# Kernel tuning notes

Hardware: AMD Instinct MI355X
Metric: run time of the kernel (lower is better)

## Reference

```python
import jax, jax.numpy as jnp
import numpy as np

N, F = 10000, 64
EDGE_PROB = 0.003  # sparse 0/1 adjacency, stored dense as in the original
LEAKY_SLOPE = 0.01
ELU_ALPHA = 1.0


def setup_inputs() -> dict:
    key = jax.random.key(0)
    ks = jax.random.split(key, 8)
    x = jax.random.normal(ks[0], (N, F), dtype=jnp.float32)
    # symmetric 0/1 adjacency (edge_index was concatenated with its flip)
    u = jax.random.uniform(ks[1], (N, N))
    A = (u < EDGE_PROB).astype(jnp.float32)
    A = jnp.maximum(A, A.T)
    dims = [F, 16, 32, 16, 32, 8]
    Ws = [jax.random.normal(ks[2 + i], (dims[i], dims[i + 1]), dtype=jnp.float32)
          * (1.0 / np.sqrt(dims[i])) for i in range(5)]
    return {"x": x, "A": A, "W0": Ws[0], "W1": Ws[1], "W2": Ws[2], "W3": Ws[3], "W4": Ws[4]}


def reference(x, A, W0, W1, W2, W3, W4):
    # layer s: temp = A @ h ; ahw = temp @ W[s] ; h = act(ahw)
    t1 = A @ x
    a1 = t1 @ W0
    h1 = jax.nn.relu(a1)

    t2 = A @ h1
    a2 = t2 @ W1
    h2 = jax.nn.silu(a2)  # swish

    t3 = A @ h2
    a3 = t3 @ W2
    h3 = jax.nn.elu(a3, alpha=ELU_ALPHA)

    t4 = A @ h3
    a4 = t4 @ W3
    h4 = jnp.where(a4 >= 0, a4, LEAKY_SLOPE * a4)  # leaky relu

    t5 = A @ h4
    a5 = t5 @ W4
    z = jax.nn.sigmoid(a5)

    # original returns (ah, ahw, z); flatten the lists into a tuple
    return (t1, t2, t3, t4, t5, a1, a2, a3, a4, a5, z)
```

## Files before the change

### kernel.cpp

```cpp
#include <hip/hip_runtime.h>
#include <math.h>

#define N_NODES 10000
#define NCH 40
#define NQ4 2500
#define CAPR 128
#define WCAP 64

typedef float f32x4 __attribute__((ext_vector_type(4)));

template <int ACT>
__device__ __forceinline__ float activate(float v) {
    if (ACT == 0) return fmaxf(v, 0.0f);
    if (ACT == 1) return v / (1.0f + __expf(-v));
    if (ACT == 2) return (v >= 0.0f) ? v : (__expf(v) - 1.0f);
    if (ACT == 3) return (v >= 0.0f) ? v : 0.01f * v;
    return 1.0f / (1.0f + __expf(-v));
}

__global__ __launch_bounds__(256) void scan_upper(
        const float* __restrict__ A,
        int* __restrict__ cu, int* __restrict__ colsU, int* __restrict__ cl) {
    __shared__ int sidx[4][WCAP];
    __shared__ int scnt[4];

    const int w    = threadIdx.x >> 6;
    const int lane = threadIdx.x & 63;
    const int row  = blockIdx.x;
    const int c0   = row >> 8;
    const int lo   = row & 255;

    const f32x4* __restrict__ arow = (const f32x4*)(A + (size_t)row * N_NODES);

    int cnt = 0;
    int c = c0 + w;
    f32x4 vc = (f32x4)(0.0f);
    if (c < NCH) {
        const int idx = c * 64 + lane;
        if (idx < NQ4) vc = __builtin_nontemporal_load(&arow[idx]);
    }
    while (c < NCH) {
        const int cn = c + 4;
        f32x4 vn = (f32x4)(0.0f);
        if (cn < NCH) {
            const int idxn = cn * 64 + lane;
            if (idxn < NQ4) vn = __builtin_nontemporal_load(&arow[idxn]);
        }
        if (c == c0) {
#pragma unroll
            for (int cc = 0; cc < 4; ++cc)
                if (4 * lane + cc < lo) vc[cc] = 0.0f;
        }
#pragma unroll
        for (int cc = 0; cc < 4; ++cc) {
            unsigned long long m = __ballot(vc[cc] != 0.0f);
            while (m) {
                const int b = __ffsll(m) - 1;
                m &= m - 1ull;
                if (lane == 0 && cnt < WCAP)
                    sidx[w][cnt] = 256 * c + 4 * b + cc;
                ++cnt;
            }
        }
        vc = vn;
        c = cn;
    }
    if (cnt > WCAP) cnt = WCAP;
    if (lane == 0) scnt[w] = cnt;
    __syncthreads();

    const int s0 = scnt[0], s1 = scnt[1], s2 = scnt[2], s3 = scnt[3];
    const int offs[4] = {0, s0, s0 + s1, s0 + s1 + s2};
    int total = s0 + s1 + s2 + s3;
    if (total > CAPR) total = CAPR;
    if (lane < scnt[w]) {
        const int p = offs[w] + lane;
        if (p < CAPR) colsU[row * CAPR + p] = sidx[w][lane];
    }
    if (threadIdx.x == 0) {
        cu[row] = total;
        cl[row] = 0;
    }
}

__global__ __launch_bounds__(256) void invert_upper(
        const int* __restrict__ cu, const int* __restrict__ colsU,
        int* __restrict__ cl, int* __restrict__ colsL) {
    const int w    = threadIdx.x >> 6;
    const int lane = threadIdx.x & 63;
    const int row  = blockIdx.x * 4 + w;

    const int n = cu[row];
    for (int k = lane; k < n; k += 64) {
        const int tgt = colsU[row * CAPR + k];
        if (tgt != row) {
            const int pos = atomicAdd(&cl[tgt], 1);
            if (pos < CAPR) colsL[tgt * CAPR + pos] = row;
        }
    }
}

__global__ __launch_bounds__(256) void sort_lower(
        int* __restrict__ cl, int* __restrict__ colsL) {
    __shared__ int sl[4][128];
    const int w    = threadIdx.x >> 6;
    const int lane = threadIdx.x & 63;
    const int row  = blockIdx.x * 4 + w;

    int n = cl[row];
    if (n > CAPR) n = CAPR;
    sl[w][lane]      = (lane < n)      ? colsL[row * CAPR + lane]      : 0x7FFFFFFF;
    sl[w][lane + 64] = (lane + 64 < n) ? colsL[row * CAPR + lane + 64] : 0x7FFFFFFF;
    __syncthreads();

    for (int size = 2; size <= 128; size <<= 1) {
        for (int stride = size >> 1; stride > 0; stride >>= 1) {
            const int i = ((lane & ~(stride - 1)) << 1) | (lane & (stride - 1));
            const int j = i | stride;
            const int a = sl[w][i], b = sl[w][j];
            const bool asc = (i & size) == 0;
            const bool doswap = asc ? (a > b) : (a < b);
            if (doswap) { sl[w][i] = b; sl[w][j] = a; }
            __syncthreads();
        }
    }

    if (lane < n)      colsL[row * CAPR + lane]      = sl[w][lane];
    if (lane + 64 < n) colsL[row * CAPR + lane + 64] = sl[w][lane + 64];
    if (lane == 0) cl[row] = n;
}

template <int FIN, int FOUT, int ACT>
__global__ __launch_bounds__(256) void layer_fused(
        const int* __restrict__ cl, const int* __restrict__ colsL,
        const int* __restrict__ cu, const int* __restrict__ colsU,
        const float* __restrict__ h_in, const float* __restrict__ W,
        float* __restrict__ t_out, float* __restrict__ a_out,
        float* __restrict__ h_out) {
    constexpr int G = 64 / FIN;
    __shared__ float tls[4][FIN];
    const int w    = threadIdx.x >> 6;
    const int lane = threadIdx.x & 63;
    const int row  = blockIdx.x * 4 + w;

    const int f = lane % FIN;
    const int g = lane / FIN;
    const int dl = cl[row];
    const int du = cu[row];
    const int* __restrict__ crowL = colsL + row * CAPR;
    const int* __restrict__ crowU = colsU + row * CAPR;

    float acc = 0.0f;
#pragma unroll 4
    for (int k = g; k < dl; k += G)
        acc += h_in[crowL[k] * FIN + f];
#pragma unroll 4
    for (int k = g; k < du; k += G)
        acc += h_in[crowU[k] * FIN + f];
#pragma unroll
    for (int off = FIN; off < 64; off <<= 1)
        acc += __shfl_xor(acc, off);
    if (g == 0) {
        t_out[row * FIN + f] = acc;
        tls[w][f] = acc;
    }
    __syncthreads();

    constexpr int NQP = 64 / FOUT;
    constexpr int K   = FIN / NQP;
    const int o = lane % FOUT, q = lane / FOUT;
    float a = 0.0f;
#pragma unroll
    for (int i = 0; i < K; ++i) {
        const int ff = q * K + i;
        a += tls[w][ff] * W[ff * FOUT + o];
    }
#pragma unroll
    for (int off = FOUT; off < 64; off <<= 1)
        a += __shfl_xor(a, off);
    if (q == 0) {
        a_out[row * FOUT + o] = a;
        h_out[row * FOUT + o] = activate<ACT>(a);
    }
}

extern "C" void kernel_launch(void* const* d_in, const int* in_sizes, int n_in,
                              void* d_out, int out_size, void* d_ws, size_t ws_size,
                              hipStream_t stream) {
    const float* x  = (const float*)d_in[0];
    const float* A  = (const float*)d_in[1];
    const float* W0 = (const float*)d_in[2];
    const float* W1 = (const float*)d_in[3];
    const float* W2 = (const float*)d_in[4];
    const float* W3 = (const float*)d_in[5];
    const float* W4 = (const float*)d_in[6];

    float* out = (float*)d_out;
    float* t1 = out + 0;
    float* t2 = out + 640000;
    float* t3 = out + 800000;
    float* t4 = out + 1120000;
    float* t5 = out + 1280000;
    float* a1 = out + 1600000;
    float* a2 = out + 1760000;
    float* a3 = out + 2080000;
    float* a4 = out + 2240000;
    float* a5 = out + 2560000;
    float* z  = out + 2640000;

    char* ws = (char*)d_ws;
    int*   cu    = (int*)ws;
    int*   cl    = (int*)(ws + (size_t)1 * 1024 * 1024);
    int*   colsU = (int*)(ws + (size_t)2 * 1024 * 1024);
    int*   colsL = (int*)(ws + (size_t)8 * 1024 * 1024);
    float* hA    = (float*)(ws + (size_t)14 * 1024 * 1024);
    float* hB    = (float*)(ws + (size_t)16 * 1024 * 1024);

    scan_upper<<<N_NODES, 256, 0, stream>>>(A, cu, colsU, cl);

    invert_upper<<<2500, 256, 0, stream>>>(cu, colsU, cl, colsL);

    sort_lower<<<2500, 256, 0, stream>>>(cl, colsL);

    layer_fused<64, 16, 0><<<2500, 256, 0, stream>>>(cl, colsL, cu, colsU,
                                                     x, W0, t1, a1, hA);
    layer_fused<16, 32, 1><<<2500, 256, 0, stream>>>(cl, colsL, cu, colsU,
                                                     hA, W1, t2, a2, hB);
    layer_fused<32, 16, 2><<<2500, 256, 0, stream>>>(cl, colsL, cu, colsU,
                                                     hB, W2, t3, a3, hA);
    layer_fused<16, 32, 3><<<2500, 256, 0, stream>>>(cl, colsL, cu, colsU,
                                                     hA, W3, t4, a4, hB);
    layer_fused<32, 8, 4><<<2500, 256, 0, stream>>>(cl, colsL, cu, colsU,
                                                    hB, W4, t5, a5, z);
}
```

Baseline: 140.1 us.

## Fuse adjacency inversion into scan and first-layer gather into sort; vectorize gathers

Merges the upper-triangle scan with the transpose/inversion step, so lower-neighbour lists are built by atomics straight from shared memory. A small kernel now zeroes the counters beforehand. Sorting the lower lists is fused with the first layer's aggregation and weight multiply, and all layer gathers switch to float4 loads. This removes two kernel launches and the re-read of colsU. The cost is heavier kernels and atomics running alongside the A scan.

```diff
diff --git a/kernel.cpp b/kernel.cpp
--- a/kernel.cpp
+++ b/kernel.cpp
@@ -18,9 +18,15 @@
     return 1.0f / (1.0f + __expf(-v));
 }
 
-__global__ __launch_bounds__(256) void scan_upper(
+__global__ void zero_cl(int* __restrict__ cl) {
+    const int i = blockIdx.x * blockDim.x + threadIdx.x;
+    if (i < N_NODES) cl[i] = 0;
+}
+
+__global__ __launch_bounds__(256) void scan_upper_inv(
         const float* __restrict__ A,
-        int* __restrict__ cu, int* __restrict__ colsU, int* __restrict__ cl) {
+        int* __restrict__ cu, int* __restrict__ colsU,
+        int* __restrict__ cl, int* __restrict__ colsL) {
     __shared__ int sidx[4][WCAP];
     __shared__ int scnt[4];
 
@@ -73,36 +79,29 @@
     const int offs[4] = {0, s0, s0 + s1, s0 + s1 + s2};
     int total = s0 + s1 + s2 + s3;
     if (total > CAPR) total = CAPR;
-    if (lane < scnt[w]) {
+
+    const int mycnt = scnt[w];
+    if (lane < mycnt) {
         const int p = offs[w] + lane;
-        if (p < CAPR) colsU[row * CAPR + p] = sidx[w][lane];
-    }
-    if (threadIdx.x == 0) {
-        cu[row] = total;
-        cl[row] = 0;
-    }
-}
-
-__global__ __launch_bounds__(256) void invert_upper(
-        const int* __restrict__ cu, const int* __restrict__ colsU,
-        int* __restrict__ cl, int* __restrict__ colsL) {
-    const int w    = threadIdx.x >> 6;
-    const int lane = threadIdx.x & 63;
-    const int row  = blockIdx.x * 4 + w;
-
-    const int n = cu[row];
-    for (int k = lane; k < n; k += 64) {
-        const int tgt = colsU[row * CAPR + k];
+        const int tgt = sidx[w][lane];
+        if (p < CAPR) colsU[row * CAPR + p] = tgt;
         if (tgt != row) {
             const int pos = atomicAdd(&cl[tgt], 1);
             if (pos < CAPR) colsL[tgt * CAPR + pos] = row;
         }
     }
-}
-
-__global__ __launch_bounds__(256) void sort_lower(
-        int* __restrict__ cl, int* __restrict__ colsL) {
-    __shared__ int sl[4][128];
+    if (threadIdx.x == 0) cu[row] = total;
+}
+
+__global__ __launch_bounds__(256) void sort_gather_l1(
+        const float* __restrict__ x, const float* __restrict__ W0,
+        int* __restrict__ cl, int* __restrict__ colsL,
+        const int* __restrict__ cu, const int* __restrict__ colsU,
+        float* __restrict__ t1, float* __restrict__ a1,
+        float* __restrict__ h1) {
+    __shared__ int   sl[4][128];
+    __shared__ float st[4][64];
+
     const int w    = threadIdx.x >> 6;
     const int lane = threadIdx.x & 63;
     const int row  = blockIdx.x * 4 + w;
@@ -128,6 +127,52 @@
     if (lane < n)      colsL[row * CAPR + lane]      = sl[w][lane];
     if (lane + 64 < n) colsL[row * CAPR + lane + 64] = sl[w][lane + 64];
     if (lane == 0) cl[row] = n;
+
+    const int du = cu[row];
+    const int dt = n + du;
+    const f32x4* __restrict__ x4 = (const f32x4*)x;
+    const int f4 = lane & 15;
+    const int g  = lane >> 4;
+
+    f32x4 acc = (f32x4)(0.0f);
+    int k = g;
+    for (; k + 12 < dt; k += 16) {
+        const int j0 = (k      < n) ? sl[w][k]      : colsU[row * CAPR + k - n];
+        const int j1 = (k + 4  < n) ? sl[w][k + 4]  : colsU[row * CAPR + k + 4 - n];
+        const int j2 = (k + 8  < n) ? sl[w][k + 8]  : colsU[row * CAPR + k + 8 - n];
+        const int j3 = (k + 12 < n) ? sl[w][k + 12] : colsU[row * CAPR + k + 12 - n];
+        acc += x4[j0 * 16 + f4];
+        acc += x4[j1 * 16 + f4];
+        acc += x4[j2 * 16 + f4];
+        acc += x4[j3 * 16 + f4];
+    }
+    for (; k < dt; k += 4) {
+        const int j = (k < n) ? sl[w][k] : colsU[row * CAPR + k - n];
+        acc += x4[j * 16 + f4];
+    }
+#pragma unroll
+    for (int cc = 0; cc < 4; ++cc) {
+        acc[cc] += __shfl_xor(acc[cc], 16);
+        acc[cc] += __shfl_xor(acc[cc], 32);
+    }
+    if (g == 0) {
+        *(f32x4*)&st[w][f4 * 4] = acc;
+        *(f32x4*)&t1[row * 64 + f4 * 4] = acc;
+    }
+
+    const int o = lane & 15, q = lane >> 4;
+    float a = 0.0f;
+#pragma unroll
+    for (int i = 0; i < 16; ++i) {
+        const int ff = q * 16 + i;
+        a += st[w][ff] * W0[ff * 16 + o];
+    }
+    a += __shfl_xor(a, 16);
+    a += __shfl_xor(a, 32);
+    if (q == 0) {
+        a1[row * 16 + o] = a;
+        h1[row * 16 + o] = activate<0>(a);
+    }
 }
 
 template <int FIN, int FOUT, int ACT>
@@ -137,32 +182,37 @@
         const float* __restrict__ h_in, const float* __restrict__ W,
         float* __restrict__ t_out, float* __restrict__ a_out,
         float* __restrict__ h_out) {
-    constexpr int G = 64 / FIN;
+    constexpr int LPR = FIN / 4;
+    constexpr int G   = 64 / LPR;
     __shared__ float tls[4][FIN];
     const int w    = threadIdx.x >> 6;
     const int lane = threadIdx.x & 63;
     const int row  = blockIdx.x * 4 + w;
 
-    const int f = lane % FIN;
-    const int g = lane / FIN;
-    const int dl = cl[row];
+    const int f4 = lane % LPR;
+    const int g  = lane / LPR;
+    int dl = cl[row]; if (dl > CAPR) dl = CAPR;
     const int du = cu[row];
     const int* __restrict__ crowL = colsL + row * CAPR;
     const int* __restrict__ crowU = colsU + row * CAPR;
-
-    float acc = 0.0f;
+    const f32x4* __restrict__ h4 = (const f32x4*)h_in;
+
+    f32x4 acc = (f32x4)(0.0f);
 #pragma unroll 4
     for (int k = g; k < dl; k += G)
-        acc += h_in[crowL[k] * FIN + f];
+        acc += h4[crowL[k] * LPR + f4];
 #pragma unroll 4
     for (int k = g; k < du; k += G)
-        acc += h_in[crowU[k] * FIN + f];
-#pragma unroll
-    for (int off = FIN; off < 64; off <<= 1)
-        acc += __shfl_xor(acc, off);
+        acc += h4[crowU[k] * LPR + f4];
+#pragma unroll
+    for (int off = LPR; off < 64; off <<= 1) {
+#pragma unroll
+        for (int cc = 0; cc < 4; ++cc)
+            acc[cc] += __shfl_xor(acc[cc], off);
+    }
     if (g == 0) {
-        t_out[row * FIN + f] = acc;
-        tls[w][f] = acc;
+        *(f32x4*)&tls[w][f4 * 4] = acc;
+        *(f32x4*)&t_out[row * FIN + f4 * 4] = acc;
     }
     __syncthreads();
 
@@ -216,14 +266,13 @@
     float* hA    = (float*)(ws + (size_t)14 * 1024 * 1024);
     float* hB    = (float*)(ws + (size_t)16 * 1024 * 1024);
 
-    scan_upper<<<N_NODES, 256, 0, stream>>>(A, cu, colsU, cl);
-
-    invert_upper<<<2500, 256, 0, stream>>>(cu, colsU, cl, colsL);
-
-    sort_lower<<<2500, 256, 0, stream>>>(cl, colsL);
-
-    layer_fused<64, 16, 0><<<2500, 256, 0, stream>>>(cl, colsL, cu, colsU,
-                                                     x, W0, t1, a1, hA);
+    zero_cl<<<40, 256, 0, stream>>>(cl);
+
+    scan_upper_inv<<<N_NODES, 256, 0, stream>>>(A, cu, colsU, cl, colsL);
+
+    sort_gather_l1<<<2500, 256, 0, stream>>>(x, W0, cl, colsL, cu, colsU,
+                                             t1, a1, hA);
+
     layer_fused<16, 32, 1><<<2500, 256, 0, stream>>>(cl, colsL, cu, colsU,
                                                      hA, W1, t2, a2, hB);
     layer_fused<32, 16, 2><<<2500, 256, 0, stream>>>(cl, colsL, cu, colsU,
```

New measurement: 116.2 us. -17.1%, faster.

## Fuse adjacency scan with transpose scatter, drop lower sort, vectorize gather

Applied to the files above, without the earlier changes.

Merges the upper-triangle scan and the inversion into one kernel. Each block scans a short row paired with a long row to balance work, then scatters lower-triangle entries with atomics straight from shared memory. The bitonic sort of lower neighbor lists is removed, so neighbor order in the sum becomes nondeterministic, which can change floating-point rounding. A small kernel now zeros the counters, and the layer aggregation gathers neighbor features as float4 vectors with fewer shuffles.

```diff
diff --git a/kernel.cpp b/kernel.cpp
--- a/kernel.cpp
+++ b/kernel.cpp
@@ -18,18 +18,16 @@
     return 1.0f / (1.0f + __expf(-v));
 }
 
-__global__ __launch_bounds__(256) void scan_upper(
-        const float* __restrict__ A,
-        int* __restrict__ cu, int* __restrict__ colsU, int* __restrict__ cl) {
-    __shared__ int sidx[4][WCAP];
-    __shared__ int scnt[4];
-
-    const int w    = threadIdx.x >> 6;
-    const int lane = threadIdx.x & 63;
-    const int row  = blockIdx.x;
-    const int c0   = row >> 8;
-    const int lo   = row & 255;
-
+__global__ void zero_cl(int* __restrict__ cl) {
+    const int i = blockIdx.x * blockDim.x + threadIdx.x;
+    if (i < N_NODES) cl[i] = 0;
+}
+
+__device__ __forceinline__ void scan_row(
+        const float* __restrict__ A, int row, int w, int lane,
+        int (* __restrict__ sidx)[WCAP], int* __restrict__ scnt) {
+    const int c0 = row >> 8;
+    const int lo = row & 255;
     const f32x4* __restrict__ arow = (const f32x4*)(A + (size_t)row * N_NODES);
 
     int cnt = 0;
@@ -67,67 +65,47 @@
     }
     if (cnt > WCAP) cnt = WCAP;
     if (lane == 0) scnt[w] = cnt;
-    __syncthreads();
-
+}
+
+__device__ __forceinline__ void epilogue_row(
+        int row, int w, int lane,
+        const int (* __restrict__ sidx)[WCAP], const int* __restrict__ scnt,
+        int* __restrict__ cu, int* __restrict__ colsU,
+        int* __restrict__ cl, int* __restrict__ colsL) {
     const int s0 = scnt[0], s1 = scnt[1], s2 = scnt[2], s3 = scnt[3];
     const int offs[4] = {0, s0, s0 + s1, s0 + s1 + s2};
     int total = s0 + s1 + s2 + s3;
     if (total > CAPR) total = CAPR;
+
     if (lane < scnt[w]) {
         const int p = offs[w] + lane;
-        if (p < CAPR) colsU[row * CAPR + p] = sidx[w][lane];
-    }
-    if (threadIdx.x == 0) {
-        cu[row] = total;
-        cl[row] = 0;
-    }
-}
-
-__global__ __launch_bounds__(256) void invert_upper(
-        const int* __restrict__ cu, const int* __restrict__ colsU,
-        int* __restrict__ cl, int* __restrict__ colsL) {
-    const int w    = threadIdx.x >> 6;
-    const int lane = threadIdx.x & 63;
-    const int row  = blockIdx.x * 4 + w;
-
-    const int n = cu[row];
-    for (int k = lane; k < n; k += 64) {
-        const int tgt = colsU[row * CAPR + k];
+        const int tgt = sidx[w][lane];
+        if (p < CAPR) colsU[row * CAPR + p] = tgt;
         if (tgt != row) {
             const int pos = atomicAdd(&cl[tgt], 1);
             if (pos < CAPR) colsL[tgt * CAPR + pos] = row;
         }
     }
-}
-
-__global__ __launch_bounds__(256) void sort_lower(
+    if (threadIdx.x == 0) cu[row] = total;
+}
+
+__global__ __launch_bounds__(256) void scan_pair(
+        const float* __restrict__ A,
+        int* __restrict__ cu, int* __restrict__ colsU,
         int* __restrict__ cl, int* __restrict__ colsL) {
-    __shared__ int sl[4][128];
+    __shared__ int sidx[2][4][WCAP];
+    __shared__ int scnt[2][4];
+
     const int w    = threadIdx.x >> 6;
     const int lane = threadIdx.x & 63;
-    const int row  = blockIdx.x * 4 + w;
-
-    int n = cl[row];
-    if (n > CAPR) n = CAPR;
-    sl[w][lane]      = (lane < n)      ? colsL[row * CAPR + lane]      : 0x7FFFFFFF;
-    sl[w][lane + 64] = (lane + 64 < n) ? colsL[row * CAPR + lane + 64] : 0x7FFFFFFF;
+    const int rowA = blockIdx.x;
+    const int rowB = N_NODES - 1 - blockIdx.x;
+
+    scan_row(A, rowA, w, lane, sidx[0], scnt[0]);
+    scan_row(A, rowB, w, lane, sidx[1], scnt[1]);
     __syncthreads();
-
-    for (int size = 2; size <= 128; size <<= 1) {
-        for (int stride = size >> 1; stride > 0; stride >>= 1) {
-            const int i = ((lane & ~(stride - 1)) << 1) | (lane & (stride - 1));
-            const int j = i | stride;
-            const int a = sl[w][i], b = sl[w][j];
-            const bool asc = (i & size) == 0;
-            const bool doswap = asc ? (a > b) : (a < b);
-            if (doswap) { sl[w][i] = b; sl[w][j] = a; }
-            __syncthreads();
-        }
-    }
-
-    if (lane < n)      colsL[row * CAPR + lane]      = sl[w][lane];
-    if (lane + 64 < n) colsL[row * CAPR + lane + 64] = sl[w][lane + 64];
-    if (lane == 0) cl[row] = n;
+    epilogue_row(rowA, w, lane, sidx[0], scnt[0], cu, colsU, cl, colsL);
+    epilogue_row(rowB, w, lane, sidx[1], scnt[1], cu, colsU, cl, colsL);
 }
 
 template <int FIN, int FOUT, int ACT>
@@ -137,32 +115,37 @@
         const float* __restrict__ h_in, const float* __restrict__ W,
         float* __restrict__ t_out, float* __restrict__ a_out,
         float* __restrict__ h_out) {
-    constexpr int G = 64 / FIN;
+    constexpr int LPR = FIN / 4;
+    constexpr int G   = 64 / LPR;
     __shared__ float tls[4][FIN];
     const int w    = threadIdx.x >> 6;
     const int lane = threadIdx.x & 63;
     const int row  = blockIdx.x * 4 + w;
 
-    const int f = lane % FIN;
-    const int g = lane / FIN;
-    const int dl = cl[row];
+    const int f4 = lane % LPR;
+    const int g  = lane / LPR;
+    int dl = cl[row]; if (dl > CAPR) dl = CAPR;
     const int du = cu[row];
     const int* __restrict__ crowL = colsL + row * CAPR;
     const int* __restrict__ crowU = colsU + row * CAPR;
-
-    float acc = 0.0f;
+    const f32x4* __restrict__ h4 = (const f32x4*)h_in;
+
+    f32x4 acc = (f32x4)(0.0f);
 #pragma unroll 4
     for (int k = g; k < dl; k += G)
-        acc += h_in[crowL[k] * FIN + f];
+        acc += h4[crowL[k] * LPR + f4];
 #pragma unroll 4
     for (int k = g; k < du; k += G)
-        acc += h_in[crowU[k] * FIN + f];
-#pragma unroll
-    for (int off = FIN; off < 64; off <<= 1)
-        acc += __shfl_xor(acc, off);
+        acc += h4[crowU[k] * LPR + f4];
+#pragma unroll
+    for (int off = LPR; off < 64; off <<= 1) {
+#pragma unroll
+        for (int cc = 0; cc < 4; ++cc)
+            acc[cc] += __shfl_xor(acc[cc], off);
+    }
     if (g == 0) {
-        t_out[row * FIN + f] = acc;
-        tls[w][f] = acc;
+        *(f32x4*)&tls[w][f4 * 4] = acc;
+        *(f32x4*)&t_out[row * FIN + f4 * 4] = acc;
     }
     __syncthreads();
 
@@ -216,11 +199,9 @@
     float* hA    = (float*)(ws + (size_t)14 * 1024 * 1024);
     float* hB    = (float*)(ws + (size_t)16 * 1024 * 1024);
 
-    scan_upper<<<N_NODES, 256, 0, stream>>>(A, cu, colsU, cl);
-
-    invert_upper<<<2500, 256, 0, stream>>>(cu, colsU, cl, colsL);
-
-    sort_lower<<<2500, 256, 0, stream>>>(cl, colsL);
+    zero_cl<<<40, 256, 0, stream>>>(cl);
+
+    scan_pair<<<N_NODES / 2, 256, 0, stream>>>(A, cu, colsU, cl, colsL);
 
     layer_fused<64, 16, 0><<<2500, 256, 0, stream>>>(cl, colsL, cu, colsU,
                                                      x, W0, t1, a1, hA);
```

After: 114.3 us. 1.23x faster.
